# Kernel optimization log

Measured on AMD Instinct MI355X. Metric: run time of the kernel, lower is better.

The kernel has to match this reference:

```python
import jax, jax.numpy as jnp
import numpy as np

B, S, D, H = 2, 2048, 512, 8


def setup_inputs() -> dict:
    key = jax.random.key(0)
    ks = jax.random.split(key, 9)
    scale = 1.0 / np.sqrt(D)
    x = jax.random.normal(ks[0], (B, S, D), dtype=jnp.float32)
    # Per-head full-width projections, stacked over heads: [H, D, D]
    Wq = jax.random.normal(ks[1], (H, D, D), dtype=jnp.float32) * scale
    Wk = jax.random.normal(ks[2], (H, D, D), dtype=jnp.float32) * scale
    Wv = jax.random.normal(ks[3], (H, D, D), dtype=jnp.float32) * scale
    bq = jax.random.normal(ks[4], (H, D), dtype=jnp.float32) * 0.01
    bk = jax.random.normal(ks[5], (H, D), dtype=jnp.float32) * 0.01
    bv = jax.random.normal(ks[6], (H, D), dtype=jnp.float32) * 0.01
    Wo = jax.random.normal(ks[7], (H * D, D), dtype=jnp.float32) * (1.0 / np.sqrt(H * D))
    bo = jax.random.normal(ks[8], (D,), dtype=jnp.float32) * 0.01
    return {"x": x, "Wq": Wq, "bq": bq, "Wk": Wk, "bk": bk, "Wv": Wv, "bv": bv, "Wo": Wo, "bo": bo}


def reference(x, Wq, bq, Wk, bk, Wv, bv, Wo, bo):
    # Batched per-head projections: [B,S,D] x [H,D,E] -> [B,H,S,E]
    q = jnp.einsum('bsd,hde->bhse', x, Wq) + bq[None, :, None, :]
    k = jnp.einsum('bsd,hde->bhse', x, Wk) + bk[None, :, None, :]
    v = jnp.einsum('bsd,hde->bhse', x, Wv) + bv[None, :, None, :]
    # NOTE: original module has NO 1/sqrt(d) scaling
    scores = jnp.einsum('bhse,bhte->bhst', q, k)  # [B,H,S,S]
    attn = jax.nn.softmax(scores, axis=-1)
    out = jnp.einsum('bhst,bhte->bhse', attn, v)  # [B,H,S,D]
    # Concat heads along feature dim: [B,S,H*D]
    cat = out.transpose(0, 2, 1, 3).reshape(B, S, H * D)
    return cat @ Wo + bo
```

## Files before the change

### kernel.cpp

```cpp
#include <hip/hip_runtime.h>

typedef _Float16 f16;
typedef _Float16 f16x8 __attribute__((ext_vector_type(8)));
typedef float f32x4 __attribute__((ext_vector_type(4)));

#define B_ 2
#define S_ 2048
#define D_ 512
#define H_ 8

__device__ inline void async_ld16(const void* g, void* l) {
  __builtin_amdgcn_global_load_lds((__attribute__((address_space(1))) void*)(g),
                                   (__attribute__((address_space(3))) void*)(l),
                                   16, 0, 0);
}

__device__ inline unsigned fmap(float f) {
  unsigned u = __float_as_uint(f);
  return (u & 0x80000000u) ? ~u : (u | 0x80000000u);
}
__device__ inline float funmap(unsigned k) {
  return (k & 0x80000000u) ? __uint_as_float(k ^ 0x80000000u) : __uint_as_float(~k);
}

__global__ __launch_bounds__(256) void cvt_f16(const float* __restrict__ src,
                                               f16* __restrict__ dst, long n) {
  long i = (long)blockIdx.x * 256 + threadIdx.x;
  if (i >= n) return;
  dst[i] = (f16)src[i];
}

__global__ __launch_bounds__(256) void transpose_f32(const float* __restrict__ src,
                                                     f16* __restrict__ dst, int R, int C) {
  __shared__ float t[32][33];
  size_t zoff = (size_t)blockIdx.z * R * C;
  const float* s = src + zoff;
  int tx = threadIdx.x;
  int ty = threadIdx.y;
  int c0 = blockIdx.x * 32, r0 = blockIdx.y * 32;
#pragma unroll
  for (int i = 0; i < 4; ++i)
    t[ty + i * 8][tx] = s[(size_t)(r0 + ty + i * 8) * C + c0 + tx];
  __syncthreads();
#pragma unroll
  for (int i = 0; i < 4; ++i)
    dst[zoff + (size_t)(c0 + ty + i * 8) * R + r0 + tx] = (f16)t[tx][ty + i * 8];
}

__global__ __launch_bounds__(256) void reduce_out(const float* __restrict__ part,
                                                  const float* __restrict__ bo,
                                                  float* __restrict__ out, long n, int nslab) {
  long i = (long)blockIdx.x * 256 + threadIdx.x;
  if (i >= n) return;
  float v = bo[i & (D_ - 1)];
  for (int s = 0; s < nslab; ++s) v += part[(long)s * n + i];
  out[i] = v;
}

struct GemmArgs {
  const f16 *A, *Bm;
  void* C;
  const float* bias;
  unsigned* Mout;
  int K, lda, ldb, ldc;
  int zbase, NG, PBG;
  long sAp, sAb, sAg, sAz;
  long sBp, sBb, sBg, sBz;
  long sCp, sCb, sCg, sCz;
  long sbp, sbb, sbg, sbz;
  long sMz;
};

template <typename OutT, int BIAS, bool RMAX>
__global__ __launch_bounds__(256) void gemm_nt(GemmArgs p) {
  int zloc = blockIdx.z;
  int zi = p.zbase + zloc;
  int pp = zi / p.PBG; int rz = zi - pp * p.PBG;
  int bb = rz / p.NG;  int g = rz - bb * p.NG;
  const f16* A  = p.A + (pp * p.sAp + bb * p.sAb + g * p.sAg + (long)zloc * p.sAz);
  const f16* Bm = p.Bm + (pp * p.sBp + bb * p.sBb + g * p.sBg + (long)zloc * p.sBz);
  OutT* C = (OutT*)p.C + (pp * p.sCp + bb * p.sCb + g * p.sCg + (long)zloc * p.sCz);
  const float* bias = nullptr;
  if (BIAS) bias = p.bias + (pp * p.sbp + bb * p.sbb + g * p.sbg + (long)zloc * p.sbz);
  unsigned* Mz = RMAX ? (p.Mout + (long)zloc * p.sMz) : nullptr;

  __shared__ f16 lA[4096];
  __shared__ f16 lB[4096];

  int tid = threadIdx.x;
  int lane = tid & 63;
  int w = tid >> 6;
  int wm = (w >> 1) << 6;
  int wn = (w & 1) << 6;
  long bm = (long)blockIdx.y * 128;
  long bn = (long)blockIdx.x * 128;

  f32x4 acc[4][4] = {};
  int qd = lane >> 4;
  int fr = lane & 15;

  int q0 = tid, q1 = tid + 256;
  int r0s = q0 >> 2, c0s = (q0 & 3) ^ ((r0s >> 1) & 3);
  int r1s = q1 >> 2, c1s = (q1 & 3) ^ ((r1s >> 1) & 3);

  for (int k0 = 0; k0 < p.K; k0 += 32) {
    long oa0 = (bm + r0s) * (long)p.lda + (k0 + c0s * 8);
    long oa1 = (bm + r1s) * (long)p.lda + (k0 + c1s * 8);
    long ob0 = (bn + r0s) * (long)p.ldb + (k0 + c0s * 8);
    long ob1 = (bn + r1s) * (long)p.ldb + (k0 + c1s * 8);
    __syncthreads();
    async_ld16(A + oa0,  lA + (size_t)q0 * 8);
    async_ld16(A + oa1,  lA + (size_t)q1 * 8);
    async_ld16(Bm + ob0, lB + (size_t)q0 * 8);
    async_ld16(Bm + ob1, lB + (size_t)q1 * 8);
    __syncthreads();

    f16x8 ah[4], bh[4];
#pragma unroll
    for (int i = 0; i < 4; ++i) {
      int m = wm + i * 16 + fr;
      ah[i] = *(const f16x8*)(lA + ((size_t)m * 4 + (qd ^ ((m >> 1) & 3))) * 8);
      int n = wn + i * 16 + fr;
      bh[i] = *(const f16x8*)(lB + ((size_t)n * 4 + (qd ^ ((n >> 1) & 3))) * 8);
    }
#pragma unroll
    for (int i = 0; i < 4; ++i)
#pragma unroll
      for (int j = 0; j < 4; ++j)
        acc[i][j] = __builtin_amdgcn_mfma_f32_16x16x32_f16(ah[i], bh[j], acc[i][j], 0, 0, 0);
  }

  int rr0 = (lane >> 4) * 4;
#pragma unroll
  for (int i = 0; i < 4; ++i) {
#pragma unroll
    for (int j = 0; j < 4; ++j) {
#pragma unroll
      for (int r = 0; r < 4; ++r) {
        long row = bm + wm + i * 16 + rr0 + r;
        long col = bn + wn + j * 16 + fr;
        float v = acc[i][j][r];
        if (BIAS == 1) v += bias[col];
        if (BIAS == 2) v += bias[row];
        C[row * (long)p.ldc + col] = (OutT)v;
      }
    }
  }
  if (RMAX) {
#pragma unroll
    for (int i = 0; i < 4; ++i) {
#pragma unroll
      for (int r = 0; r < 4; ++r) {
        float pm = fmaxf(fmaxf(acc[i][0][r], acc[i][1][r]),
                         fmaxf(acc[i][2][r], acc[i][3][r]));
        pm = fmaxf(pm, __shfl_xor(pm, 1, 64));
        pm = fmaxf(pm, __shfl_xor(pm, 2, 64));
        pm = fmaxf(pm, __shfl_xor(pm, 4, 64));
        pm = fmaxf(pm, __shfl_xor(pm, 8, 64));
        if (fr == 0) atomicMax(Mz + (bm + wm + i * 16 + rr0 + r), fmap(pm));
      }
    }
  }
}

struct PvArgs {
  const f16* S; const unsigned* M; const f16* V; f16* C;
  int ldc, zbase, NG;
  long sVz, sCb, sCg;
};
__global__ __launch_bounds__(256) void pv_flash(PvArgs p) {
  int zloc = blockIdx.z;
  int zi = p.zbase + zloc;
  int bb = zi / p.NG; int g = zi - bb * p.NG;
  const f16* Sm = p.S + (long)zloc * S_ * S_;
  const unsigned* Mz = p.M + (long)zloc * S_;
  const f16* V = p.V + (long)zloc * p.sVz;
  f16* C = p.C + bb * p.sCb + g * p.sCg;

  __shared__ f16 lS[64 * 32];
  __shared__ f16 lP[64 * 32];
  __shared__ f16 lV[256 * 32];

  int tid = threadIdx.x;
  int lane = tid & 63;
  int w = tid >> 6;
  long bm = (long)blockIdx.y * 64;
  long bn = (long)blockIdx.x * 256;
  int e0 = w << 6;

  int qd = lane >> 4;
  int fr = lane & 15;

  f32x4 acc[4][4] = {};
  f32x4 lacc[4] = {};
  f16x8 ones;
#pragma unroll
  for (int j = 0; j < 8; ++j) ones[j] = (f16)1.0f;

  int rs = tid >> 2, cs = (tid & 3) ^ ((rs >> 1) & 3);
  float mrow = funmap(Mz[bm + rs]);

  for (int k0 = 0; k0 < S_; k0 += 32) {
    __syncthreads();
    async_ld16(Sm + (bm + rs) * (long)S_ + (k0 + cs * 8), lS + (size_t)tid * 8);
#pragma unroll
    for (int j = 0; j < 4; ++j) {
      int q = j * 256 + tid;
      int rv = q >> 2, cv = (q & 3) ^ ((rv >> 1) & 3);
      async_ld16(V + (bn + rv) * (long)S_ + (k0 + cv * 8), lV + (size_t)q * 8);
    }
    __syncthreads();

    {
      f16x8 sv = *(const f16x8*)(lS + (size_t)tid * 8);
      f16x8 pv;
#pragma unroll
      for (int j = 0; j < 8; ++j) pv[j] = (f16)__expf((float)sv[j] - mrow);
      *(f16x8*)(lP + (size_t)tid * 8) = pv;
    }
    __syncthreads();

    f16x8 ah[4], bh[4];
#pragma unroll
    for (int i = 0; i < 4; ++i) {
      int m = i * 16 + fr;
      ah[i] = *(const f16x8*)(lP + ((size_t)m * 4 + (qd ^ ((m >> 1) & 3))) * 8);
    }
#pragma unroll
    for (int j = 0; j < 4; ++j) {
      int n = e0 + j * 16 + fr;
      bh[j] = *(const f16x8*)(lV + ((size_t)n * 4 + (qd ^ ((n >> 1) & 3))) * 8);
    }
#pragma unroll
    for (int i = 0; i < 4; ++i) {
      lacc[i] = __builtin_amdgcn_mfma_f32_16x16x32_f16(ah[i], ones, lacc[i], 0, 0, 0);
#pragma unroll
      for (int j = 0; j < 4; ++j)
        acc[i][j] = __builtin_amdgcn_mfma_f32_16x16x32_f16(ah[i], bh[j], acc[i][j], 0, 0, 0);
    }
  }

  int rr0 = (lane >> 4) * 4;
#pragma unroll
  for (int i = 0; i < 4; ++i) {
    float inv[4];
#pragma unroll
    for (int r = 0; r < 4; ++r) inv[r] = 1.0f / lacc[i][r];
#pragma unroll
    for (int j = 0; j < 4; ++j) {
#pragma unroll
      for (int r = 0; r < 4; ++r) {
        long row = bm + i * 16 + rr0 + r;
        long col = bn + e0 + j * 16 + fr;
        C[row * (long)p.ldc + col] = (f16)(acc[i][j][r] * inv[r]);
      }
    }
  }
}

extern "C" void kernel_launch(void* const* d_in, const int* in_sizes, int n_in,
                              void* d_out, int out_size, void* d_ws, size_t ws_size,
                              hipStream_t stream) {
  const float* x  = (const float*)d_in[0];
  const float* Wq = (const float*)d_in[1];
  const float* bq = (const float*)d_in[2];
  const float* Wk = (const float*)d_in[3];
  const float* bk = (const float*)d_in[4];
  const float* Wv = (const float*)d_in[5];
  const float* bv = (const float*)d_in[6];
  const float* Wo = (const float*)d_in[7];
  const float* bo = (const float*)d_in[8];
  float* out = (float*)d_out;

  auto al = [](size_t v) { return (v + 255) & ~(size_t)255; };
  const size_t eX = (size_t)B_ * S_ * D_;
  const size_t eW = (size_t)H_ * D_ * D_;
  const size_t eSS = (size_t)S_ * S_;
  const long SD = (long)S_ * D_;
  const long DD = (long)D_ * D_;
  const long DS = (long)D_ * S_;

  size_t fixed = al(eX * 2) + al(2 * eW * 2) + al(eW * 2) + al(eW * 2)
               + al(2ULL * H_ * D_ * 4);
  int NB = 1, GH = 1, GS = 1; bool found = false;
  for (int nb = 2; nb >= 1 && !found; --nb)
    for (int gh = 8; gh >= 1 && !found; gh >>= 1)
      for (int gs = nb * gh; gs >= 1 && !found; gs >>= 1) {
        size_t need = fixed + al((size_t)nb * S_ * H_ * D_ * 2)
                    + al(2ULL * nb * gh * S_ * D_ * 2)
                    + al((size_t)nb * gh * D_ * S_ * 2)
                    + al(2ULL * nb * SD * 4)
                    + al((size_t)gs * eSS * 2) + al((size_t)gs * S_ * 4);
        if (need <= ws_size) { NB = nb; GH = gh; GS = gs; found = true; }
      }

  char* p0 = (char*)d_ws;
  size_t off = 0;
  f16* xh    = (f16*)(p0 + off); off += al(eX * 2);
  f16* wqk   = (f16*)(p0 + off); off += al(2 * eW * 2);
  f16* wv    = (f16*)(p0 + off); off += al(eW * 2);
  f16* wo    = (f16*)(p0 + off); off += al(eW * 2);
  float* bqk = (float*)(p0 + off); off += al(2ULL * H_ * D_ * 4);
  f16* catb  = (f16*)(p0 + off); off += al((size_t)NB * S_ * H_ * D_ * 2);
  f16* qk    = (f16*)(p0 + off); off += al(2ULL * NB * GH * S_ * D_ * 2);
  f16* vT    = (f16*)(p0 + off); off += al((size_t)NB * GH * D_ * S_ * 2);
  float* opart = (float*)(p0 + off); off += al(2ULL * NB * SD * 4);
  f16* scores = (f16*)(p0 + off); off += al((size_t)GS * eSS * 2);
  unsigned* rowmax = (unsigned*)(p0 + off);

  cvt_f16<<<dim3((unsigned)((eX + 255) / 256)), 256, 0, stream>>>(x, xh, (long)eX);
  dim3 tb(32, 8, 1);
  transpose_f32<<<dim3(16, 16, H_), tb, 0, stream>>>(Wq, wqk, D_, D_);
  transpose_f32<<<dim3(16, 16, H_), tb, 0, stream>>>(Wk, wqk + eW, D_, D_);
  transpose_f32<<<dim3(16, 16, H_), tb, 0, stream>>>(Wv, wv, D_, D_);
  transpose_f32<<<dim3(16, 128, 1), tb, 0, stream>>>(Wo, wo, H_ * D_, D_);
  hipMemcpyAsync(bqk, bq, (size_t)H_ * D_ * 4, hipMemcpyDeviceToDevice, stream);
  hipMemcpyAsync(bqk + H_ * D_, bk, (size_t)H_ * D_ * 4, hipMemcpyDeviceToDevice, stream);

  for (int b0 = 0; b0 < B_; b0 += NB) {
    for (int h0 = 0; h0 < H_; h0 += GH) {
      {
        GemmArgs a{};
        a.A = xh + (long)b0 * SD;
        a.Bm = wqk + (long)h0 * DD;
        a.C = qk; a.bias = bqk + (long)h0 * D_;
        a.K = D_; a.lda = D_; a.ldb = D_; a.ldc = D_;
        a.zbase = 0; a.NG = GH; a.PBG = NB * GH;
        a.sAb = SD;
        a.sBp = (long)H_ * DD; a.sBg = DD;
        a.sCz = SD;
        a.sbp = (long)H_ * D_; a.sbg = D_;
        gemm_nt<f16, 1, false><<<dim3(4, 16, 2 * NB * GH), 256, 0, stream>>>(a);
      }
      {
        GemmArgs a{};
        a.A = wv + (long)h0 * DD; a.Bm = xh + (long)b0 * SD;
        a.C = vT; a.bias = bv + (long)h0 * D_;
        a.K = D_; a.lda = D_; a.ldb = D_; a.ldc = S_;
        a.zbase = 0; a.NG = GH; a.PBG = NB * GH;
        a.sAg = DD;
        a.sBb = SD;
        a.sCz = DS;
        a.sbg = D_;
        gemm_nt<f16, 2, false><<<dim3(16, 4, NB * GH), 256, 0, stream>>>(a);
      }
      for (int g0 = 0; g0 < NB * GH; g0 += GS) {
        hipMemsetAsync(rowmax, 0, (size_t)GS * S_ * 4, stream);
        {
          GemmArgs a{};
          a.A = qk + (long)g0 * SD;
          a.Bm = qk + ((long)NB * GH + g0) * SD;
          a.C = scores; a.Mout = rowmax;
          a.K = D_; a.lda = D_; a.ldb = D_; a.ldc = S_;
          a.zbase = g0; a.NG = GH; a.PBG = NB * GH;
          a.sAz = SD; a.sBz = SD; a.sCz = (long)eSS; a.sMz = S_;
          gemm_nt<f16, 0, true><<<dim3(16, 16, GS), 256, 0, stream>>>(a);
        }
        {
          PvArgs a{};
          a.S = scores; a.M = rowmax; a.V = vT + (long)g0 * DS;
          a.C = catb + (long)h0 * D_;
          a.ldc = H_ * D_; a.zbase = g0; a.NG = GH;
          a.sVz = DS; a.sCb = (long)S_ * H_ * D_; a.sCg = D_;
          pv_flash<<<dim3(2, S_ / 64, GS), 256, 0, stream>>>(a);
        }
      }
    }
    {
      GemmArgs a{};
      a.A = catb; a.Bm = wo;
      a.C = opart;
      a.K = 2048; a.lda = H_ * D_; a.ldb = H_ * D_; a.ldc = D_;
      a.zbase = 0; a.NG = 2; a.PBG = NB * 2;
      a.sAb = (long)S_ * H_ * D_; a.sAg = 2048;
      a.sBg = 2048;
      a.sCb = SD; a.sCg = (long)NB * SD;
      gemm_nt<float, 0, false><<<dim3(4, 16, NB * 2), 256, 0, stream>>>(a);
    }
    reduce_out<<<dim3((unsigned)(((long)NB * SD + 255) / 256)), 256, 0, stream>>>(
        opart, bo, out + (long)b0 * SD, (long)NB * SD, 2);
  }
}
```

Before: 555.7 us.

## Fuse exp into QK^T epilogue with per-tile local max and rescale in PV

The QK^T GEMM epilogue now computes a per-128-column-tile row max through shared memory, writes exp(s - local max) as f16, and stores the local max per tile. The PV kernel no longer exponentiates scores. It loads them directly into the MFMA staging buffer and rescales each A fragment by exp(local max - global max). This removes a shared-memory pass, one barrier and the per-element exp from the PV inner loop. The cost is an extra synchronisation in the GEMM epilogue, a small extra buffer, and precision risk from storing unnormalised f16 values relative to local rather than global maxima.

```diff
diff --git a/kernel.cpp b/kernel.cpp
--- a/kernel.cpp
+++ b/kernel.cpp
@@ -62,16 +62,17 @@
   void* C;
   const float* bias;
   unsigned* Mout;
+  float* Mloc;
   int K, lda, ldb, ldc;
   int zbase, NG, PBG;
   long sAp, sAb, sAg, sAz;
   long sBp, sBb, sBg, sBz;
   long sCp, sCb, sCg, sCz;
   long sbp, sbb, sbg, sbz;
-  long sMz;
+  long sMz, sMlz;
 };
 
-template <typename OutT, int BIAS, bool RMAX>
+template <typename OutT, int BIAS, bool PEXP>
 __global__ __launch_bounds__(256) void gemm_nt(GemmArgs p) {
   int zloc = blockIdx.z;
   int zi = p.zbase + zloc;
@@ -82,10 +83,11 @@
   OutT* C = (OutT*)p.C + (pp * p.sCp + bb * p.sCb + g * p.sCg + (long)zloc * p.sCz);
   const float* bias = nullptr;
   if (BIAS) bias = p.bias + (pp * p.sbp + bb * p.sbb + g * p.sbg + (long)zloc * p.sbz);
-  unsigned* Mz = RMAX ? (p.Mout + (long)zloc * p.sMz) : nullptr;
+  unsigned* Mz = PEXP ? (p.Mout + (long)zloc * p.sMz) : nullptr;
 
   __shared__ f16 lA[4096];
   __shared__ f16 lB[4096];
+  __shared__ float lMx[PEXP ? 256 : 1];
 
   int tid = threadIdx.x;
   int lane = tid & 63;
@@ -130,41 +132,61 @@
         acc[i][j] = __builtin_amdgcn_mfma_f32_16x16x32_f16(ah[i], bh[j], acc[i][j], 0, 0, 0);
   }
 
-  int rr0 = (lane >> 4) * 4;
-#pragma unroll
-  for (int i = 0; i < 4; ++i) {
-#pragma unroll
-    for (int j = 0; j < 4; ++j) {
+  int rr0 = qd * 4;
+  if (PEXP) {
+#pragma unroll
+    for (int i = 0; i < 4; ++i) {
 #pragma unroll
       for (int r = 0; r < 4; ++r) {
-        long row = bm + wm + i * 16 + rr0 + r;
-        long col = bn + wn + j * 16 + fr;
-        float v = acc[i][j][r];
-        if (BIAS == 1) v += bias[col];
-        if (BIAS == 2) v += bias[row];
-        C[row * (long)p.ldc + col] = (OutT)v;
+        float v = fmaxf(fmaxf(acc[i][0][r], acc[i][1][r]),
+                        fmaxf(acc[i][2][r], acc[i][3][r]));
+        v = fmaxf(v, __shfl_xor(v, 1, 64));
+        v = fmaxf(v, __shfl_xor(v, 2, 64));
+        v = fmaxf(v, __shfl_xor(v, 4, 64));
+        v = fmaxf(v, __shfl_xor(v, 8, 64));
+        if (fr == 0) lMx[(w & 1) * 128 + wm + i * 16 + rr0 + r] = v;
+      }
+    }
+    __syncthreads();
+#pragma unroll
+    for (int i = 0; i < 4; ++i) {
+#pragma unroll
+      for (int r = 0; r < 4; ++r) {
+        int rl = wm + i * 16 + rr0 + r;
+        float ml = fmaxf(lMx[rl], lMx[128 + rl]);
+        long row = bm + rl;
+#pragma unroll
+        for (int j = 0; j < 4; ++j) {
+          long col = bn + wn + j * 16 + fr;
+          ((f16*)C)[row * (long)p.ldc + col] = (f16)__expf(acc[i][j][r] - ml);
+        }
+        if ((w & 1) == 0 && fr == 0) {
+          p.Mloc[(long)zloc * p.sMlz + (long)blockIdx.x * S_ + row] = ml;
+          atomicMax(Mz + row, fmap(ml));
+        }
+      }
+    }
+  } else {
+#pragma unroll
+    for (int i = 0; i < 4; ++i) {
+#pragma unroll
+      for (int j = 0; j < 4; ++j) {
+#pragma unroll
+        for (int r = 0; r < 4; ++r) {
+          long row = bm + wm + i * 16 + rr0 + r;
+          long col = bn + wn + j * 16 + fr;
+          float v = acc[i][j][r];
+          if (BIAS == 1) v += bias[col];
+          if (BIAS == 2) v += bias[row];
+          C[row * (long)p.ldc + col] = (OutT)v;
+        }
       }
     }
   }
-  if (RMAX) {
-#pragma unroll
-    for (int i = 0; i < 4; ++i) {
-#pragma unroll
-      for (int r = 0; r < 4; ++r) {
-        float pm = fmaxf(fmaxf(acc[i][0][r], acc[i][1][r]),
-                         fmaxf(acc[i][2][r], acc[i][3][r]));
-        pm = fmaxf(pm, __shfl_xor(pm, 1, 64));
-        pm = fmaxf(pm, __shfl_xor(pm, 2, 64));
-        pm = fmaxf(pm, __shfl_xor(pm, 4, 64));
-        pm = fmaxf(pm, __shfl_xor(pm, 8, 64));
-        if (fr == 0) atomicMax(Mz + (bm + wm + i * 16 + rr0 + r), fmap(pm));
-      }
-    }
-  }
 }
 
 struct PvArgs {
-  const f16* S; const unsigned* M; const f16* V; f16* C;
+  const f16* S; const unsigned* M; const float* Ml; const f16* V; f16* C;
   int ldc, zbase, NG;
   long sVz, sCb, sCg;
 };
@@ -174,10 +196,10 @@
   int bb = zi / p.NG; int g = zi - bb * p.NG;
   const f16* Sm = p.S + (long)zloc * S_ * S_;
   const unsigned* Mz = p.M + (long)zloc * S_;
+  const float* Ml = p.Ml + (long)zloc * 16 * S_;
   const f16* V = p.V + (long)zloc * p.sVz;
   f16* C = p.C + bb * p.sCb + g * p.sCg;
 
-  __shared__ f16 lS[64 * 32];
   __shared__ f16 lP[64 * 32];
   __shared__ f16 lV[256 * 32];
 
@@ -197,12 +219,22 @@
 #pragma unroll
   for (int j = 0; j < 8; ++j) ones[j] = (f16)1.0f;
 
+  float mg[4];
+#pragma unroll
+  for (int i = 0; i < 4; ++i) mg[i] = funmap(Mz[bm + i * 16 + fr]);
+  f16 al16[4];
+
   int rs = tid >> 2, cs = (tid & 3) ^ ((rs >> 1) & 3);
-  float mrow = funmap(Mz[bm + rs]);
 
   for (int k0 = 0; k0 < S_; k0 += 32) {
+    if ((k0 & 127) == 0) {
+      int cb = k0 >> 7;
+#pragma unroll
+      for (int i = 0; i < 4; ++i)
+        al16[i] = (f16)__expf(Ml[cb * S_ + bm + i * 16 + fr] - mg[i]);
+    }
     __syncthreads();
-    async_ld16(Sm + (bm + rs) * (long)S_ + (k0 + cs * 8), lS + (size_t)tid * 8);
+    async_ld16(Sm + (bm + rs) * (long)S_ + (k0 + cs * 8), lP + (size_t)tid * 8);
 #pragma unroll
     for (int j = 0; j < 4; ++j) {
       int q = j * 256 + tid;
@@ -211,20 +243,13 @@
     }
     __syncthreads();
 
-    {
-      f16x8 sv = *(const f16x8*)(lS + (size_t)tid * 8);
-      f16x8 pv;
-#pragma unroll
-      for (int j = 0; j < 8; ++j) pv[j] = (f16)__expf((float)sv[j] - mrow);
-      *(f16x8*)(lP + (size_t)tid * 8) = pv;
-    }
-    __syncthreads();
-
     f16x8 ah[4], bh[4];
 #pragma unroll
     for (int i = 0; i < 4; ++i) {
       int m = i * 16 + fr;
       ah[i] = *(const f16x8*)(lP + ((size_t)m * 4 + (qd ^ ((m >> 1) & 3))) * 8);
+#pragma unroll
+      for (int j = 0; j < 8; ++j) ah[i][j] *= al16[i];
     }
 #pragma unroll
     for (int j = 0; j < 4; ++j) {
@@ -290,7 +315,8 @@
                     + al(2ULL * nb * gh * S_ * D_ * 2)
                     + al((size_t)nb * gh * D_ * S_ * 2)
                     + al(2ULL * nb * SD * 4)
-                    + al((size_t)gs * eSS * 2) + al((size_t)gs * S_ * 4);
+                    + al((size_t)gs * eSS * 2) + al((size_t)gs * S_ * 4)
+                    + al((size_t)gs * 16 * S_ * 4);
         if (need <= ws_size) { NB = nb; GH = gh; GS = gs; found = true; }
       }
 
@@ -306,7 +332,8 @@
   f16* vT    = (f16*)(p0 + off); off += al((size_t)NB * GH * D_ * S_ * 2);
   float* opart = (float*)(p0 + off); off += al(2ULL * NB * SD * 4);
   f16* scores = (f16*)(p0 + off); off += al((size_t)GS * eSS * 2);
-  unsigned* rowmax = (unsigned*)(p0 + off);
+  unsigned* rowmax = (unsigned*)(p0 + off); off += al((size_t)GS * S_ * 4);
+  float* mloc = (float*)(p0 + off);
 
   cvt_f16<<<dim3((unsigned)((eX + 255) / 256)), 256, 0, stream>>>(x, xh, (long)eX);
   dim3 tb(32, 8, 1);
@@ -350,15 +377,16 @@
           GemmArgs a{};
           a.A = qk + (long)g0 * SD;
           a.Bm = qk + ((long)NB * GH + g0) * SD;
-          a.C = scores; a.Mout = rowmax;
+          a.C = scores; a.Mout = rowmax; a.Mloc = mloc;
           a.K = D_; a.lda = D_; a.ldb = D_; a.ldc = S_;
           a.zbase = g0; a.NG = GH; a.PBG = NB * GH;
           a.sAz = SD; a.sBz = SD; a.sCz = (long)eSS; a.sMz = S_;
+          a.sMlz = 16L * S_;
           gemm_nt<f16, 0, true><<<dim3(16, 16, GS), 256, 0, stream>>>(a);
         }
         {
           PvArgs a{};
-          a.S = scores; a.M = rowmax; a.V = vT + (long)g0 * DS;
+          a.S = scores; a.M = rowmax; a.Ml = mloc; a.V = vT + (long)g0 * DS;
           a.C = catb + (long)h0 * D_;
           a.ldc = H_ * D_; a.zbase = g0; a.NG = GH;
           a.sVz = DS; a.sCb = (long)S_ * H_ * D_; a.sCg = D_;
```

New measurement: 534.0 us. 1.04x faster.
